# Kernel tuning notes

Hardware: AMD Instinct MI355X
Metric: run time of the kernel (lower is better)

The kernel has to match this reference:

```python
import jax, jax.numpy as jnp
import numpy as np

U = 256      # lstm_unit / embedding_fc_unit
V = 100000   # word vocab
WD = 300     # word embedding dim
PD = 64      # pos embedding dim
AD = 64      # action embedding dim
P = 50       # pos vocab
NA = 164     # 4 + 4*dep_num actions
B, T, K, L, S, A, DQ = 64, 128, 4, 128, 64, 64, 32
FORGET_BIAS = 1.0


def lstm_step(x, c, h, W, b):
    z = jnp.concatenate([x, h], -1) @ W + b
    i, j, f, o = jnp.split(z, 4, -1)
    nc = c * jax.nn.sigmoid(f + FORGET_BIAS) + jax.nn.sigmoid(i) * jnp.tanh(j)
    nh = jnp.tanh(nc) * jax.nn.sigmoid(o)
    return nc, nh


def run_lstm(xs, length, W, b):
    # xs: [B, L, D]; TF dynamic_rnn semantics: state frozen and output zeroed past length.
    Bn, Ln, _ = xs.shape
    u = W.shape[1] // 4
    def step(carry, tx):
        c, h = carry
        t, x = tx
        nc, nh = lstm_step(x, c, h, W, b)
        m = (t < length)[:, None]
        return (jnp.where(m, nc, c), jnp.where(m, nh, h)), jnp.where(m, nh, 0.0)
    init = (jnp.zeros((Bn, u), xs.dtype), jnp.zeros((Bn, u), xs.dtype))
    (cf, hf), outs = jax.lax.scan(step, init, (jnp.arange(Ln), jnp.swapaxes(xs, 0, 1)))
    return jnp.swapaxes(outs, 0, 1), (cf, hf)


def reverse_seq(xs, length):
    # tf.reverse_sequence: reverse first `length` steps, leave the rest in place.
    Ln = xs.shape[1]
    t = jnp.arange(Ln)[None, :]
    rev = jnp.where(t < length[:, None], length[:, None] - 1 - t, t)
    return jnp.take_along_axis(xs, rev[:, :, None], axis=1)


def forward(tree_word_id, tree_pos_id, token_word_id, token_pos_id, history_action_id,
            buff_top_id, deque_word_id, deque_pos_id, deque_length, children_order,
            stack_order, stack_length, token_length, history_action_length,
            word_emb, pos_emb, act_emb, wd_W, wd_b, tree_W, tree_b,
            stack0_W, stack0_b, stack1_W, stack1_b,
            fw0_W, fw0_b, bw0_W, bw0_b, fw1_W, fw1_b, bw1_W, bw1_b,
            act0_W, act0_b, act1_W, act1_b, dq0_W, dq0_b, dq1_W, dq1_b,
            fin_W, fin_b):
    Bn = tree_word_id.shape[0]

    def embed(wid, pid):
        e = jnp.concatenate([word_emb[wid], pos_emb[pid]], -1)
        return jax.nn.relu(e @ wd_W + wd_b)

    tree_e = embed(tree_word_id, tree_pos_id)       # [B, T, U]
    token_e = embed(token_word_id, token_pos_id)    # [B, L, U]
    deque_e = embed(deque_word_id, deque_pos_id)    # [B, DQ, U]
    hist_e = act_emb[history_action_id]             # [B, A, AD]

    # ---- tree LSTM over children structure ----
    Tn = tree_e.shape[1]
    Kn = children_order.shape[2]
    batch_col = jnp.arange(Bn)[:, None]
    H0 = jnp.zeros((Tn + 1, Bn, U), tree_e.dtype)
    C0 = jnp.zeros((Tn + 1, Bn, U), tree_e.dtype)

    def body(carry, i):
        H, C = carry
        idx = children_order[:, i]            # [B, K] indices into slots 0..i
        h = H[idx, batch_col]                 # [B, K, U]
        c = C[idx, batch_col]
        x = tree_e[:, i]                      # [B, U]
        hj = h.sum(1)
        ijo = jnp.concatenate([x, hj], -1) @ tree_W[:, :3 * U] + tree_b[:3 * U]
        xk = jnp.broadcast_to(x[:, None, :], (Bn, Kn, x.shape[-1]))
        f = jnp.concatenate([xk, h], -1) @ tree_W[:, 3 * U:] + tree_b[3 * U:]   # [B, K, U]
        ig, jg, og = jnp.split(ijo, 3, -1)
        nc = (c * jax.nn.sigmoid(f + FORGET_BIAS)).sum(1) + jax.nn.sigmoid(ig) * jnp.tanh(jg)
        nh = jnp.tanh(nc) * jax.nn.sigmoid(og)
        return (H.at[i + 1].set(nh), C.at[i + 1].set(nc)), None

    (H, _), _ = jax.lax.scan(body, (H0, C0), jnp.arange(Tn))
    stack_embedded = H[stack_order, batch_col]      # [B, S, U]

    # ---- stack LSTM (2-layer) ----
    o0, _ = run_lstm(stack_embedded, stack_length, stack0_W, stack0_b)
    _, (_, stack_h) = run_lstm(o0, stack_length, stack1_W, stack1_b)

    # ---- buff bi-LSTM (2 stacked bidirectional layers) ----
    fw0_o, _ = run_lstm(token_e, token_length, fw0_W, fw0_b)
    bw0_o, _ = run_lstm(reverse_seq(token_e, token_length), token_length, bw0_W, bw0_b)
    bw0_o = reverse_seq(bw0_o, token_length)
    x1 = jnp.concatenate([fw0_o, bw0_o], -1)
    fw1_o, (_, fw1_h) = run_lstm(x1, token_length, fw1_W, fw1_b)
    bw1_o, _ = run_lstm(reverse_seq(x1, token_length), token_length, bw1_W, bw1_b)
    bw1_o = reverse_seq(bw1_o, token_length)
    bidx = jnp.arange(Bn)
    fw_top = fw1_o[bidx, buff_top_id]
    bw_top = bw1_o[bidx, buff_top_id]
    bw_bottom = bw1_o[bidx, token_length - 1]
    buff_out = jnp.concatenate([fw1_h - fw_top, bw_top - bw_bottom], -1)

    # ---- action LSTM (2-layer) ----
    a0, _ = run_lstm(hist_e, history_action_length, act0_W, act0_b)
    _, (_, act_h) = run_lstm(a0, history_action_length, act1_W, act1_b)

    # ---- deque LSTM (2-layer) ----
    d0, _ = run_lstm(deque_e, deque_length, dq0_W, dq0_b)
    _, (_, dq_h) = run_lstm(d0, deque_length, dq1_W, dq1_b)

    feat = jnp.concatenate([stack_h, buff_out, act_h, dq_h], -1)   # [B, 5U]
    return jax.nn.relu(feat @ fin_W + fin_b)


def setup_inputs():
    key = jax.random.key(0)
    ks = jax.random.split(key, 48)
    r = lambda i, shape: jax.random.normal(ks[i], shape, jnp.float32) * 0.05
    ri = lambda i, shape, hi: jax.random.randint(ks[i], shape, 0, hi)
    inp = {}
    inp['tree_word_id'] = ri(0, (B, T), V)
    inp['tree_pos_id'] = ri(1, (B, T), P)
    inp['token_word_id'] = ri(2, (B, L), V)
    inp['token_pos_id'] = ri(3, (B, L), P)
    inp['history_action_id'] = ri(4, (B, A), NA)
    inp['buff_top_id'] = ri(5, (B,), L // 2)
    inp['deque_word_id'] = ri(6, (B, DQ), V)
    inp['deque_pos_id'] = ri(7, (B, DQ), P)
    inp['deque_length'] = jax.random.randint(ks[8], (B,), 1, DQ + 1)
    co = ri(9, (B, T, K), T)
    # a node may only reference already-computed children slots (<= step index)
    inp['children_order'] = jnp.minimum(co, jnp.arange(T)[None, :, None])
    inp['stack_order'] = ri(10, (B, S), T + 1)
    inp['stack_length'] = jax.random.randint(ks[11], (B,), 1, S + 1)
    inp['token_length'] = jax.random.randint(ks[12], (B,), L // 2, L + 1)
    inp['history_action_length'] = jax.random.randint(ks[13], (B,), 1, A + 1)
    inp['word_emb'] = r(14, (V, WD))
    inp['pos_emb'] = r(15, (P, PD))
    inp['act_emb'] = r(16, (NA, AD))
    inp['wd_W'] = r(17, (WD + PD, U)); inp['wd_b'] = jnp.zeros((U,))
    inp['tree_W'] = r(18, (2 * U, 4 * U)); inp['tree_b'] = jnp.zeros((4 * U,))
    inp['stack0_W'] = r(19, (2 * U, 4 * U)); inp['stack0_b'] = jnp.zeros((4 * U,))
    inp['stack1_W'] = r(20, (2 * U, 4 * U)); inp['stack1_b'] = jnp.zeros((4 * U,))
    inp['fw0_W'] = r(21, (2 * U, 4 * U)); inp['fw0_b'] = jnp.zeros((4 * U,))
    inp['bw0_W'] = r(22, (2 * U, 4 * U)); inp['bw0_b'] = jnp.zeros((4 * U,))
    inp['fw1_W'] = r(23, (3 * U, 4 * U)); inp['fw1_b'] = jnp.zeros((4 * U,))
    inp['bw1_W'] = r(24, (3 * U, 4 * U)); inp['bw1_b'] = jnp.zeros((4 * U,))
    inp['act0_W'] = r(25, (AD + U, 4 * U)); inp['act0_b'] = jnp.zeros((4 * U,))
    inp['act1_W'] = r(26, (2 * U, 4 * U)); inp['act1_b'] = jnp.zeros((4 * U,))
    inp['dq0_W'] = r(27, (2 * U, 4 * U)); inp['dq0_b'] = jnp.zeros((4 * U,))
    inp['dq1_W'] = r(28, (2 * U, 4 * U)); inp['dq1_b'] = jnp.zeros((4 * U,))
    inp['fin_W'] = r(29, (5 * U, NA)); inp['fin_b'] = jnp.zeros((NA,))
    return inp


def reference(tree_word_id, tree_pos_id, token_word_id, token_pos_id, history_action_id,
              buff_top_id, deque_word_id, deque_pos_id, deque_length, children_order,
              stack_order, stack_length, token_length, history_action_length,
              word_emb, pos_emb, act_emb, wd_W, wd_b, tree_W, tree_b,
              stack0_W, stack0_b, stack1_W, stack1_b,
              fw0_W, fw0_b, bw0_W, bw0_b, fw1_W, fw1_b, bw1_W, bw1_b,
              act0_W, act0_b, act1_W, act1_b, dq0_W, dq0_b, dq1_W, dq1_b,
              fin_W, fin_b):
    return forward(tree_word_id, tree_pos_id, token_word_id, token_pos_id, history_action_id,
                   buff_top_id, deque_word_id, deque_pos_id, deque_length, children_order,
                   stack_order, stack_length, token_length, history_action_length,
                   word_emb, pos_emb, act_emb, wd_W, wd_b, tree_W, tree_b,
                   stack0_W, stack0_b, stack1_W, stack1_b,
                   fw0_W, fw0_b, bw0_W, bw0_b, fw1_W, fw1_b, bw1_W, bw1_b,
                   act0_W, act0_b, act1_W, act1_b, dq0_W, dq0_b, dq1_W, dq1_b,
                   fin_W, fin_b)
```

## Files before the change

### kernel.cpp

```cpp
#include <hip/hip_runtime.h>
#include <hip/hip_bf16.h>
#include <hip/hip_fp16.h>
#include <cstdint>

#define BB   64
#define TT   128
#define KK   4
#define LL   128
#define SS   64
#define AA   64
#define DQN  32
#define UU   256
#define NAOUT 164
#define WDIM 300
#define PDIM 64
#define ADIM 64

#define OFF_TREE 0
#define OFF_S0   512
#define OFF_S1   1024
#define OFF_FW0  1536
#define OFF_BW0  2048
#define OFF_FW1  2560
#define OFF_BW1  3328
#define OFF_ACT0 4096
#define OFF_ACT1 4416
#define OFF_DQ0  4928
#define OFF_DQ1  5440
#define PK_ROWS_FB 5952

#define PKH_FW0  512
#define PKH_BW0  768
#define PKH_FW1  1024
#define PKH_BW1  1280
#define PKH_S0   1536
#define PKH_S1   1792
#define PKH_ACT0 2048
#define PKH_ACT1 2304
#define PKH_DQ0  2560
#define PKH_DQ1  2816
#define PK_ROWS_B 3072

typedef unsigned short ushort_t;
typedef unsigned int   uint_t;

__device__ __forceinline__ float bf2f(ushort_t s) {
    return __uint_as_float(((uint_t)s) << 16);
}
__device__ __forceinline__ ushort_t f2bf(float x) {
    __hip_bfloat16 h = __float2bfloat16(x);
    return *reinterpret_cast<ushort_t*>(&h);
}
__device__ __forceinline__ float sigm(float x) { return 1.0f / (1.0f + expf(-x)); }

__device__ __forceinline__ uint_t pack2h(float a, float b) {
    __half2 h = __floats2half2_rn(a, b);
    return *reinterpret_cast<uint_t*>(&h);
}
__device__ __forceinline__ float2 unp2h(uint_t v) {
    __half2 h = *reinterpret_cast<__half2*>(&v);
    return __half22float2(h);
}

template<bool F32>
__device__ __forceinline__ float ld1(const void* p_, size_t i) {
    if constexpr (F32) return reinterpret_cast<const float*>(p_)[i];
    else               return bf2f(reinterpret_cast<const ushort_t*>(p_)[i]);
}

struct P {
    const int *tree_word_id, *tree_pos_id, *token_word_id, *token_pos_id, *history_action_id,
              *buff_top_id, *deque_word_id, *deque_pos_id, *deque_length, *children_order,
              *stack_order, *stack_length, *token_length, *history_action_length;
    const void *word_emb, *pos_emb, *act_emb, *wd_W, *wd_b, *tree_W, *tree_b,
        *stack0_W, *stack0_b, *stack1_W, *stack1_b, *fw0_W, *fw0_b, *bw0_W, *bw0_b,
        *fw1_W, *fw1_b, *bw1_W, *bw1_b, *act0_W, *act0_b, *act1_W, *act1_b,
        *dq0_W, *dq0_b, *dq1_W, *dq1_b, *fin_W, *fin_b;
    int* flag;
    float *stack_h, *fw1_h, *fw_top, *bw_top, *bw_bottom, *act_h, *dq_h;
    float *tree_e;
    ushort_t *token_e, *deque_e, *x1;
    float *H, *C;
    float *a0_seq, *d0_seq, *s0_seq;
    uint2 *zxA, *zxB, *zxC, *zxD, *zxS;
    float4* pkf;
};

__global__ void detect_kernel(const uint_t* w, int* flag) {
    __shared__ int cnt;
    if (threadIdx.x == 0) cnt = 0;
    __syncthreads();
    int local = 0;
    for (int i = threadIdx.x; i < 256; i += 64) {
        uint_t lo = w[i] & 0xFFFFu;
        uint_t e  = (lo >> 7) & 0xFFu;
        if (lo == 0u || (e >= 0x6Cu && e <= 0x7Fu)) local++;
    }
    atomicAdd(&cnt, local);
    __syncthreads();
    if (threadIdx.x == 0) flag[0] = (cnt >= 200) ? 0 : 1;
}

__global__ void sentinel_kernel(void* out, float v) {
    if (threadIdx.x == 0) {
        reinterpret_cast<float*>(out)[0] = v;
        reinterpret_cast<__hip_bfloat16*>(out)[2] = __float2bfloat16(v);
    }
}

__global__ __launch_bounds__(256) void pack_fb_kernel(P p) {
    const bool f32 = (p.flag[0] == 1);
    const int rg = blockIdx.x;
    const int u  = threadIdx.x;
    const void* src; int r;
    if      (rg < 512)  { src = p.tree_W;   r = rg; }
    else if (rg < 1024) { src = p.stack0_W; r = rg - 512; }
    else if (rg < 1536) { src = p.stack1_W; r = rg - 1024; }
    else if (rg < 2048) { src = p.fw0_W;    r = rg - 1536; }
    else if (rg < 2560) { src = p.bw0_W;    r = rg - 2048; }
    else if (rg < 3328) { src = p.fw1_W;    r = rg - 2560; }
    else if (rg < 4096) { src = p.bw1_W;    r = rg - 3328; }
    else if (rg < 4416) { src = p.act0_W;   r = rg - 4096; }
    else if (rg < 4928) { src = p.act1_W;   r = rg - 4416; }
    else if (rg < 5440) { src = p.dq0_W;    r = rg - 4928; }
    else                { src = p.dq1_W;    r = rg - 5440; }
    const size_t ro = (size_t)r * 1024;
    float4 v;
    if (f32) {
        const float* s = reinterpret_cast<const float*>(src) + ro;
        v = make_float4(s[u], s[256 + u], s[512 + u], s[768 + u]);
    } else {
        const ushort_t* s = reinterpret_cast<const ushort_t*>(src) + ro;
        v = make_float4(bf2f(s[u]), bf2f(s[256 + u]), bf2f(s[512 + u]), bf2f(s[768 + u]));
    }
    p.pkf[(size_t)rg * 256 + u] = v;
}

__global__ __launch_bounds__(256) void pack_h_kernel(P p) {
    const bool f32 = (p.flag[0] == 1);
    const int rg = blockIdx.x;
    const int u  = threadIdx.x;
    const void* src; int r;
    if      (rg < 512)  { src = p.tree_W;   r = rg; }
    else if (rg < 768)  { src = p.fw0_W;    r = 256 + rg - 512; }
    else if (rg < 1024) { src = p.bw0_W;    r = 256 + rg - 768; }
    else if (rg < 1280) { src = p.fw1_W;    r = 512 + rg - 1024; }
    else if (rg < 1536) { src = p.bw1_W;    r = 512 + rg - 1280; }
    else if (rg < 1792) { src = p.stack0_W; r = 256 + rg - 1536; }
    else if (rg < 2048) { src = p.stack1_W; r = 256 + rg - 1792; }
    else if (rg < 2304) { src = p.act0_W;   r = 64  + rg - 2048; }
    else if (rg < 2560) { src = p.act1_W;   r = 256 + rg - 2304; }
    else if (rg < 2816) { src = p.dq0_W;    r = 256 + rg - 2560; }
    else                { src = p.dq1_W;    r = 256 + rg - 2816; }
    const size_t ro = (size_t)r * 1024;
    float4 v;
    if (f32) {
        const float* s = reinterpret_cast<const float*>(src) + ro;
        v = make_float4(s[u], s[256 + u], s[512 + u], s[768 + u]);
    } else {
        const ushort_t* s = reinterpret_cast<const ushort_t*>(src) + ro;
        v = make_float4(bf2f(s[u]), bf2f(s[256 + u]), bf2f(s[512 + u]), bf2f(s[768 + u]));
    }
    p.pkf[(size_t)rg * 256 + u] = v;
}

template<bool F32>
__device__ void embed_impl(const P& p, float* s_e) {
    const int u   = threadIdx.x;
// ... 316 lines not shown
    s_xh[512 + u] = 0.f;
    for (int t = 0; t < len; ++t) {
        const int row = is_bw ? (len - 1 - t) : t;
        const ushort_t* xr = p.x1 + ((size_t)b * LL + row) * 512;
        s_xh[u]       = bf2f(xr[u]);
        s_xh[256 + u] = bf2f(xr[256 + u]);
        __syncthreads();
        const float nh = lstm_step_f4<768>(Wp, bz, s_xh, c1);
        if (!is_bw) {
            if (t == btop) p.fw_top[b * UU + u] = nh;
        } else {
            if (t == 0)              p.bw_bottom[b * UU + u] = nh;
            if (t == len - 1 - btop) p.bw_top[b * UU + u]    = nh;
        }
        __syncthreads();
        s_xh[512 + u] = nh;
        hlast = nh;
    }
    if (!is_bw) p.fw1_h[b * UU + u] = hlast;
}

__global__ __launch_bounds__(256) void phase2_fb_kernel(P p) {
    __shared__ __align__(16) float smem[1024];
    const bool f32 = (p.flag[0] == 1);
    const int chain = blockIdx.x % 3;
    const int b     = blockIdx.x / 3;
    if (f32) {
        if (chain == 0)      run_stack_f4<true>(b, p, smem);
        else if (chain == 1) run_token_l1_f4<true>(b, p, smem, false);
        else                 run_token_l1_f4<true>(b, p, smem, true);
    } else {
        if (chain == 0)      run_stack_f4<false>(b, p, smem);
        else if (chain == 1) run_token_l1_f4<false>(b, p, smem, false);
        else                 run_token_l1_f4<false>(b, p, smem, true);
    }
}

template<bool F32, int R>
__device__ void xpre_compute(const void* __restrict__ W, const void* __restrict__ bias,
                             uint2* __restrict__ zx, int n0,
                             const float* __restrict__ s_xf, const ushort_t* __restrict__ s_xb) {
    const int u = threadIdx.x;
    const float4 bz = load_bias4<F32>(bias, u);
    for (int c = 0; c < 32; c += 8) {
        float4 acc[8];
        #pragma unroll
        for (int n = 0; n < 8; ++n) acc[n] = bz;
        for (int r0 = 0; r0 < R; r0 += 8) {
            float4 w[8];
            #pragma unroll
            for (int k = 0; k < 8; ++k) {
                const size_t ro = (size_t)(r0 + k) * 1024;
                w[k] = make_float4(ld1<F32>(W, ro + u),
                                   ld1<F32>(W, ro + 256 + u),
                                   ld1<F32>(W, ro + 512 + u),
                                   ld1<F32>(W, ro + 768 + u));
            }
            #pragma unroll
            for (int n = 0; n < 8; ++n) {
                float xv[8];
                #pragma unroll
                for (int k = 0; k < 8; ++k)
                    xv[k] = (R == 512) ? bf2f(s_xb[(size_t)(c + n) * 512 + r0 + k])
                                       : s_xf[(size_t)(c + n) * R + r0 + k];
                #pragma unroll
                for (int k = 0; k < 8; ++k) {
                    acc[n].x = fmaf(xv[k], w[k].x, acc[n].x);
                    acc[n].y = fmaf(xv[k], w[k].y, acc[n].y);
                    acc[n].z = fmaf(xv[k], w[k].z, acc[n].z);
                    acc[n].w = fmaf(xv[k], w[k].w, acc[n].w);
                }
            }
        }
        #pragma unroll
        for (int n = 0; n < 8; ++n) {
            uint2 v;
            v.x = pack2h(acc[n].x, acc[n].y);
            v.y = pack2h(acc[n].z, acc[n].w);
            zx[(size_t)(n0 + c + n) * 256 + u] = v;
        }
    }
}

template<bool F32, int STAGE>
__device__ void xpre_impl(const P& p, char* s_raw) {
    float*    s_xf = reinterpret_cast<float*>(s_raw);
    ushort_t* s_xb = reinterpret_cast<ushort_t*>(s_raw);
    const int blk = blockIdx.x;
    const int tid = threadIdx.x;

    const void* W; const void* bias; uint2* zx; int R; int kind; int n0;
    if (STAGE == 0) {
        if (blk < 256)      { W=p.fw0_W;  bias=p.fw0_b;  zx=p.zxA; R=256; kind=0; n0=blk*32; }
        else if (blk < 512) { W=p.bw0_W;  bias=p.bw0_b;  zx=p.zxB; R=256; kind=0; n0=(blk-256)*32; }
        else if (blk < 640) { W=p.act0_W; bias=p.act0_b; zx=p.zxC; R=64;  kind=3; n0=(blk-512)*32; }
        else                { W=p.dq0_W;  bias=p.dq0_b;  zx=p.zxD; R=256; kind=1; n0=(blk-640)*32; }
    } else if (STAGE == 1) {
        if (blk < 256)      { W=p.fw1_W;    bias=p.fw1_b;    zx=p.zxA; R=512; kind=2; n0=blk*32; }
        else if (blk < 512) { W=p.bw1_W;    bias=p.bw1_b;    zx=p.zxB; R=512; kind=2; n0=(blk-256)*32; }
        else if (blk < 640) { W=p.stack0_W; bias=p.stack0_b; zx=p.zxS; R=256; kind=4; n0=(blk-512)*32; }
        else if (blk < 768) { W=p.act1_W;   bias=p.act1_b;   zx=p.zxC; R=256; kind=5; n0=(blk-640)*32; }
        else                { W=p.dq1_W;    bias=p.dq1_b;    zx=p.zxD; R=256; kind=6; n0=(blk-768)*32; }
    } else {
        W=p.stack1_W; bias=p.stack1_b; zx=p.zxS; R=256; kind=7; n0=blk*32;
    }

    if (kind == 0 || kind == 1) {
        const ushort_t* src = (kind == 0 ? p.token_e : p.deque_e) + (size_t)n0 * 256;
        for (int i = tid; i < 32 * 256; i += 256) s_xf[i] = bf2f(src[i]);
    } else if (kind == 2) {
        const ushort_t* src = p.x1 + (size_t)n0 * 512;
        for (int i = tid; i < 32 * 512; i += 256) s_xb[i] = src[i];
    } else if (kind == 3) {
        const int b = n0 >> 6, t0 = n0 & 63;
        for (int i = tid; i < 32 * 64; i += 256) {
            const int t = t0 + (i >> 6), r = i & 63;
            int aid = p.history_action_id[b * AA + t];
            aid = aid < 0 ? 0 : (aid > NAOUT - 1 ? NAOUT - 1 : aid);
            s_xf[i] = ld1<F32>(p.act_emb, (size_t)aid * ADIM + r);
        }
    } else if (kind == 4) {
        const int b = n0 >> 6, t0 = n0 & 63;
        for (int i = tid; i < 32 * 256; i += 256) {
            const int t = t0 + (i >> 8), r = i & 255;
            int so = p.stack_order[b * SS + t];
            so = so < 0 ? 0 : (so > TT ? TT : so);
            s_xf[i] = p.H[((size_t)so * BB + b) * UU + r];
        }
    } else {
        const float* src = (kind == 5 ? p.a0_seq : kind == 6 ? p.d0_seq : p.s0_seq)
                         + (size_t)n0 * 256;
        for (int i = tid; i < 32 * 256; i += 256) s_xf[i] = src[i];
    }
    __syncthreads();

    if (R == 512)      xpre_compute<F32, 512>(W, bias, zx, n0, s_xf, s_xb);
    else if (R == 256) xpre_compute<F32, 256>(W, bias, zx, n0, s_xf, s_xb);
    else               xpre_compute<F32, 64 >(W, bias, zx, n0, s_xf, s_xb);
}

__global__ __launch_bounds__(256) void xpre0_kernel(P p) {
    __shared__ __align__(16) char s_raw[32768];
    if (p.flag[0] == 1) xpre_impl<true, 0>(p, s_raw);
    else                xpre_impl<false, 0>(p, s_raw);
}
__global__ __launch_bounds__(256) void xpre1_kernel(P p) {
    __shared__ __align__(16) char s_raw[32768];
    if (p.flag[0] == 1) xpre_impl<true, 1>(p, s_raw);
    else                xpre_impl<false, 1>(p, s_raw);
}
__global__ __launch_bounds__(256) void xpre2_kernel(P p) {
    __shared__ __align__(16) char s_raw[32768];
    if (p.flag[0] == 1) xpre_impl<true, 2>(p, s_raw);
    else                xpre_impl<false, 2>(p, s_raw);
}

template<bool F32>
__device__ void p1_impl(const P& p, float* smem) {
    const int chain = blockIdx.x >> 6;
    const int b     = blockIdx.x & 63;
    if (chain == 0) { run_tree_f4<F32>(b, p, smem); return; }

    const int u = threadIdx.x;
    float* s_h = smem;
    float c = 0.f;
    s_h[u] = 0.f;
    __syncthreads();

    if (chain == 1 || chain == 2) {
        const bool bw = (chain == 2);
        const int len = p.token_length[b];
        const float4* __restrict__ Wh = p.pkf + (size_t)(bw ? PKH_BW0 : PKH_FW0) * 256 + u;
        const uint2* zx = bw ? p.zxB : p.zxA;
        for (int t = 0; t < len; ++t) {
            const int row = bw ? (len - 1 - t) : t;
            const float4 bz = zx_load(zx, (size_t)b * LL + row, u);
            const float nh = lstm_step_f4<256>(Wh, bz, s_h, c);
            p.x1[((size_t)b * LL + row) * 512 + (bw ? 256 : 0) + u] = f2bf(nh);
            __syncthreads();
            s_h[u] = nh;
            __syncthreads();
        }
    } else if (chain == 3) {
        const int len = p.history_action_length[b];
        const float4* __restrict__ Wh = p.pkf + (size_t)PKH_ACT0 * 256 + u;
        for (int t = 0; t < len; ++t) {
            const float4 bz = zx_load(p.zxC, (size_t)b * AA + t, u);
            const float nh = lstm_step_f4<256>(Wh, bz, s_h, c);
            p.a0_seq[((size_t)b * AA + t) * UU + u] = nh;
            __syncthreads();
            s_h[u] = nh;
            __syncthreads();
        }
    } else {
        const int len = p.deque_length[b];
        const float4* __restrict__ Wh = p.pkf + (size_t)PKH_DQ0 * 256 + u;
        for (int t = 0; t < len; ++t) {
            const float4 bz = zx_load(p.zxD, (size_t)b * DQN + t, u);
            const float nh = lstm_step_f4<256>(Wh, bz, s_h, c);
            p.d0_seq[((size_t)b * DQN + t) * UU + u] = nh;
            __syncthreads();
            s_h[u] = nh;
            __syncthreads();
        }
    }
}

__global__ __launch_bounds__(256) void p1_kernel(P p) {
    __shared__ __align__(16) float smem[1536];
    if (p.flag[0] == 1) p1_impl<true>(p, smem);
    else                p1_impl<false>(p, smem);
}

template<bool F32>
__device__ void p2_impl(const P& p, float* smem) {
    const int chain = blockIdx.x >> 6;
    const int b     = blockIdx.x & 63;
    const int u = threadIdx.x;
    float* s_h = smem;
    float c = 0.f;
    s_h[u] = 0.f;
    __syncthreads();

    if (chain == 0) {
        const int len  = p.token_length[b];
        const int btop = p.buff_top_id[b];
        const float4* __restrict__ Wh = p.pkf + (size_t)PKH_FW1 * 256 + u;
        float hlast = 0.f;
        for (int t = 0; t < len; ++t) {
            const float4 bz = zx_load(p.zxA, (size_t)b * LL + t, u);
            const float nh = lstm_step_f4<256>(Wh, bz, s_h, c);
            if (t == btop) p.fw_top[b * UU + u] = nh;
            __syncthreads();
            s_h[u] = nh;
            __syncthreads();
            hlast = nh;
        }
        p.fw1_h[b * UU + u] = hlast;
    } else if (chain == 1) {
        const int len  = p.token_length[b];
        const int btop = p.buff_top_id[b];
        const float4* __restrict__ Wh = p.pkf + (size_t)PKH_BW1 * 256 + u;
        for (int t = 0; t < len; ++t) {
            const int row = len - 1 - t;
            const float4 bz = zx_load(p.zxB, (size_t)b * LL + row, u);
            const float nh = lstm_step_f4<256>(Wh, bz, s_h, c);
            if (t == 0)              p.bw_bottom[b * UU + u] = nh;
            if (t == len - 1 - btop) p.bw_top[b * UU + u]    = nh;
            __syncthreads();
            s_h[u] = nh;
            __syncthreads();
        }
    } else if (chain == 2) {
        const int len = p.stack_length[b];
        const float4* __restrict__ Wh = p.pkf + (size_t)PKH_S0 * 256 + u;
        for (int t = 0; t < len; ++t) {
            const float4 bz = zx_load(p.zxS, (size_t)b * SS + t, u);
            const float nh = lstm_step_f4<256>(Wh, bz, s_h, c);
            p.s0_seq[((size_t)b * SS + t) * UU + u] = nh;
            __syncthreads();
            s_h[u] = nh;
            __syncthreads();
        }
    } else if (chain == 3) {
        const int len = p.history_action_length[b];
        const float4* __restrict__ Wh = p.pkf + (size_t)PKH_ACT1 * 256 + u;
        float hlast = 0.f;
        for (int t = 0; t < len; ++t) {
            const float4 bz = zx_load(p.zxC, (size_t)b * AA + t, u);
            const float nh = lstm_step_f4<256>(Wh, bz, s_h, c);
            __syncthreads();
            s_h[u] = nh;
            __syncthreads();
            hlast = nh;
        }
        p.act_h[b * UU + u] = hlast;
    } else {
        const int len = p.deque_length[b];
        const float4* __restrict__ Wh = p.pkf + (size_t)PKH_DQ1 * 256 + u;
        float hlast = 0.f;
        for (int t = 0; t < len; ++t) {
            const float4 bz = zx_load(p.zxD, (size_t)b * DQN + t, u);
            const float nh = lstm_step_f4<256>(Wh, bz, s_h, c);
            __syncthreads();
            s_h[u] = nh;
            __syncthreads();
            hlast = nh;
        }
        p.dq_h[b * UU + u] = hlast;
    }
}

__global__ __launch_bounds__(256) void p2_kernel(P p) {
    __shared__ __align__(16) float smem[256];
    if (p.flag[0] == 1) p2_impl<true>(p, smem);
    else                p2_impl<false>(p, smem);
}

template<bool F32>
__device__ void p3_impl(const P& p, float* smem) {
    const int b = blockIdx.x;
    const int u = threadIdx.x;
    float* s_h = smem;
    float c = 0.f;
    s_h[u] = 0.f;
    __syncthreads();
    const int len = p.stack_length[b];
    const float4* __restrict__ Wh = p.pkf + (size_t)PKH_S1 * 256 + u;
    float hlast = 0.f;
    for (int t = 0; t < len; ++t) {
        const float4 bz = zx_load(p.zxS, (size_t)b * SS + t, u);
        const float nh = lstm_step_f4<256>(Wh, bz, s_h, c);
        __syncthreads();
        s_h[u] = nh;
        __syncthreads();
        hlast = nh;
    }
    p.stack_h[b * UU + u] = hlast;
}

__global__ __launch_bounds__(256) void p3_kernel(P p) {
    __shared__ __align__(16) float smem[256];
    if (p.flag[0] == 1) p3_impl<true>(p, smem);
    else                p3_impl<false>(p, smem);
}

template<bool F32>
__device__ __forceinline__ void st_out(void* out, int i, float v) {
    if constexpr (F32) reinterpret_cast<float*>(out)[i] = v;
    else               reinterpret_cast<__hip_bfloat16*>(out)[i] = __float2bfloat16(v);
}

template<bool F32>
__device__ void final_impl(const P& p, void* out, float* s_f) {
    const int b = blockIdx.x;
    const int u = threadIdx.x;
    s_f[u]        = p.stack_h[b * UU + u];
    s_f[256 + u]  = p.fw1_h[b * UU + u] - p.fw_top[b * UU + u];
    s_f[512 + u]  = p.bw_top[b * UU + u] - p.bw_bottom[b * UU + u];
    s_f[768 + u]  = p.act_h[b * UU + u];
    s_f[1024 + u] = p.dq_h[b * UU + u];
    __syncthreads();
    if (u < NAOUT) {
        float acc = ld1<F32>(p.fin_b, u);
        for (int r = 0; r < 1280; ++r)
            acc = fmaf(s_f[r], ld1<F32>(p.fin_W, (size_t)r * NAOUT + u), acc);
        acc = fmaxf(acc, 0.f);
        st_out<F32>(out, b * NAOUT + u, acc);
    }
    if (b == 0 && u == 0) {
        const uint_t POIS = 0xAAAAAAAAu;
        const uint_t* te = reinterpret_cast<const uint_t*>(p.tree_e);
        const uint_t* x1 = reinterpret_cast<const uint_t*>(p.x1);
        const uint_t* sh = reinterpret_cast<const uint_t*>(p.stack_h);
        bool te_p = true, x1_p = true;
        for (int i = 0; i < 8; ++i) { te_p &= (te[i] == POIS); x1_p &= (x1[i] == POIS); }
        bool sh_p = (sh[0] == POIS) && (sh[1] == POIS);
        float sent = 0.f;
        if (te_p)      sent = 3000.f;
        else if (x1_p) sent = 4000.f;
        else if (sh_p) sent = 5000.f;
        else if (*reinterpret_cast<const uint_t*>(p.flag) == POIS) sent = 6000.f;
        if (sent > 0.f) st_out<F32>(out, 0, sent);
    }
}

__global__ __launch_bounds__(256) void final_kernel(P p, void* out) {
    __shared__ __align__(16) float s_f[1280];
    if (p.flag[0] == 1) final_impl<true>(p, out, s_f);
    else                final_impl<false>(p, out, s_f);
}

extern "C" void kernel_launch(void* const* d_in, const int* in_sizes, int n_in,
                              void* d_out, int out_size, void* d_ws, size_t ws_size,
                              hipStream_t stream) {
    if (n_in != 43) {
        sentinel_kernel<<<1, 64, 0, stream>>>(d_out, 9000.f + (float)n_in);
        return;
    }
    if (out_size != NAOUT * BB) {
        sentinel_kernel<<<1, 64, 0, stream>>>(d_out, 8000.f);
        return;
    }

    P p;
    p.tree_word_id          = (const int*)d_in[0];
    p.tree_pos_id           = (const int*)d_in[1];
    p.token_word_id         = (const int*)d_in[2];
    p.token_pos_id          = (const int*)d_in[3];
    p.history_action_id     = (const int*)d_in[4];
    p.buff_top_id           = (const int*)d_in[5];
    p.deque_word_id         = (const int*)d_in[6];
    p.deque_pos_id          = (const int*)d_in[7];
    p.deque_length          = (const int*)d_in[8];
    p.children_order        = (const int*)d_in[9];
    p.stack_order           = (const int*)d_in[10];
    p.stack_length          = (const int*)d_in[11];
    p.token_length          = (const int*)d_in[12];
    p.history_action_length = (const int*)d_in[13];
    p.word_emb = d_in[14];
    p.pos_emb  = d_in[15];
    p.act_emb  = d_in[16];
    p.wd_W     = d_in[17];
    p.wd_b     = d_in[18];
    p.tree_W   = d_in[19];
    p.tree_b   = d_in[20];
    p.stack0_W = d_in[21];
    p.stack0_b = d_in[22];
    p.stack1_W = d_in[23];
    p.stack1_b = d_in[24];
    p.fw0_W    = d_in[25];
    p.fw0_b    = d_in[26];
    p.bw0_W    = d_in[27];
    p.bw0_b    = d_in[28];
    p.fw1_W    = d_in[29];
    p.fw1_b    = d_in[30];
    p.bw1_W    = d_in[31];
    p.bw1_b    = d_in[32];
    p.act0_W   = d_in[33];
    p.act0_b   = d_in[34];
    p.act1_W   = d_in[35];
    p.act1_b   = d_in[36];
    p.dq0_W    = d_in[37];
    p.dq0_b    = d_in[38];
    p.dq1_W    = d_in[39];
    p.dq1_b    = d_in[40];
    p.fin_W    = d_in[41];
    p.fin_b    = d_in[42];

    char* base = (char*)d_ws;

    size_t off = 0;
    p.flag = (int*)(base + off);           off += 256;
    p.stack_h   = (float*)(base + off);    off += (size_t)BB * UU * 4;
    p.fw1_h     = (float*)(base + off);    off += (size_t)BB * UU * 4;
    p.fw_top    = (float*)(base + off);    off += (size_t)BB * UU * 4;
    p.bw_top    = (float*)(base + off);    off += (size_t)BB * UU * 4;
    p.bw_bottom = (float*)(base + off);    off += (size_t)BB * UU * 4;
    p.act_h     = (float*)(base + off);    off += (size_t)BB * UU * 4;
    p.dq_h      = (float*)(base + off);    off += (size_t)BB * UU * 4;
    p.tree_e  = (float*)(base + off);      off += (size_t)BB * TT * UU * 4;
    p.token_e = (ushort_t*)(base + off);   off += (size_t)BB * LL * UU * 2;
    p.deque_e = (ushort_t*)(base + off);   off += (size_t)BB * DQN * UU * 2;
    p.x1      = (ushort_t*)(base + off);   off += (size_t)BB * LL * 512 * 2;
    p.a0_seq  = (float*)(base + off);      off += (size_t)BB * AA * UU * 4;
    p.d0_seq  = (float*)(base + off);      off += (size_t)BB * DQN * UU * 4;
    p.s0_seq  = (float*)(base + off);      off += (size_t)BB * SS * UU * 4;
    p.H       = (float*)(base + off);      off += (size_t)(TT + 1) * BB * UU * 4;
    p.C       = (float*)(base + off);      off += (size_t)(TT + 1) * BB * UU * 4;
    p.zxA     = (uint2*)(base + off);      off += (size_t)BB * LL * UU * 8;
    p.zxB     = (uint2*)(base + off);      off += (size_t)BB * LL * UU * 8;
    p.zxC     = (uint2*)(base + off);      off += (size_t)BB * AA * UU * 8;
    p.zxD     = (uint2*)(base + off);      off += (size_t)BB * DQN * UU * 8;
    p.zxS     = (uint2*)(base + off);      off += (size_t)BB * SS * UU * 8;
    p.pkf     = (float4*)(base + off);     off += (size_t)PK_ROWS_B * 256 * 16;
    const size_t planB_size = off;

    if (ws_size >= planB_size) {
        detect_kernel<<<1, 64, 0, stream>>>((const uint_t*)d_in[14], p.flag);
        pack_h_kernel<<<dim3(PK_ROWS_B), dim3(256), 0, stream>>>(p);
        embed_kernel<<<dim3(BB * TT + BB * LL + BB * DQN), dim3(256), 0, stream>>>(p);
        xpre0_kernel<<<dim3(704), dim3(256), 0, stream>>>(p);
        p1_kernel<<<dim3(5 * BB), dim3(256), 0, stream>>>(p);
        xpre1_kernel<<<dim3(832), dim3(256), 0, stream>>>(p);
        p2_kernel<<<dim3(5 * BB), dim3(256), 0, stream>>>(p);
        xpre2_kernel<<<dim3(128), dim3(256), 0, stream>>>(p);
        p3_kernel<<<dim3(BB), dim3(256), 0, stream>>>(p);
        final_kernel<<<dim3(BB), dim3(256), 0, stream>>>(p, d_out);
        return;
    }

    off = 0;
    p.flag = (int*)(base + off);           off += 16;
    p.stack_h   = (float*)(base + off);    off += (size_t)BB * UU * 4;
    p.fw1_h     = (float*)(base + off);    off += (size_t)BB * UU * 4;
    p.fw_top    = (float*)(base + off);    off += (size_t)BB * UU * 4;
    p.bw_top    = (float*)(base + off);    off += (size_t)BB * UU * 4;
    p.bw_bottom = (float*)(base + off);    off += (size_t)BB * UU * 4;
    p.act_h     = (float*)(base + off);    off += (size_t)BB * UU * 4;
    p.dq_h      = (float*)(base + off);    off += (size_t)BB * UU * 4;
    p.tree_e  = (float*)(base + off);      off += (size_t)BB * TT * UU * 4;
    p.token_e = (ushort_t*)(base + off);   off += (size_t)BB * LL * UU * 2;
    p.deque_e = (ushort_t*)(base + off);   off += (size_t)BB * DQN * UU * 2;
    p.x1      = (ushort_t*)(base + off);   off += (size_t)BB * LL * 512 * 2;
    p.H       = (float*)(base + off);      off += (size_t)(TT + 1) * BB * UU * 4;
    p.C       = (float*)(base + off);      off += (size_t)(TT + 1) * BB * UU * 4;
    p.pkf     = (float4*)(base + off);     off += (size_t)PK_ROWS_FB * 256 * 16;
    p.a0_seq = p.d0_seq = p.s0_seq = (float*)base;
    p.zxA = p.zxB = p.zxC = p.zxD = p.zxS = (uint2*)base;

    if (ws_size < off) {
        sentinel_kernel<<<1, 64, 0, stream>>>(d_out, 7000.f + (float)(ws_size >> 20));
        return;
    }

    detect_kernel<<<1, 64, 0, stream>>>((const uint_t*)d_in[14], p.flag);
    pack_fb_kernel<<<dim3(PK_ROWS_FB), dim3(256), 0, stream>>>(p);
    embed_kernel<<<dim3(BB * TT + BB * LL + BB * DQN), dim3(256), 0, stream>>>(p);
    phase1_fb_kernel<<<dim3(4 * BB), dim3(256), 0, stream>>>(p);
    phase2_fb_kernel<<<dim3(3 * BB), dim3(256), 0, stream>>>(p);
    final_kernel<<<dim3(BB), dim3(256), 0, stream>>>(p, d_out);
}
```

Baseline: 6.336 ms.

## Split recurrent LSTM chains into per-timestep grid launches across units and batch

Replaces the persistent per-batch-row recurrent kernels (one block per sequence running all timesteps) with one kernel launch per timestep. Each launch spreads the hidden units and batch rows over 256 blocks, with hidden and cell state kept in global double-buffered arrays. The tree LSTM's input projection is moved into the xpre0 GEMM stage (new zxT buffer), so each tree step only does the recurrent part. The aim is to use many more CUs per step and share weight loads across batch rows. The cost is hundreds of kernel launches and a global-memory round trip for state on every step.

```diff
diff --git a/kernel.cpp b/kernel.cpp
--- a/kernel.cpp
+++ b/kernel.cpp
@@ -83,7 +83,10 @@
     float *H, *C;
     float *a0_seq, *d0_seq, *s0_seq;
     uint2 *zxA, *zxB, *zxC, *zxD, *zxS;
+    float4* zxT;
     float4* pkf;
+    float *hs;
+    float *cs;
 };
 
 __global__ void detect_kernel(const uint_t* w, int* flag) {
@@ -566,6 +569,46 @@
     }
 }
 
+template<bool F32>
+__device__ void xpre_tree_compute(const void* __restrict__ W, const void* __restrict__ bias,
+                                  float4* __restrict__ zxT, int n0,
+                                  const float* __restrict__ s_xf) {
+    const int u = threadIdx.x;
+    const float4 bz = make_float4(ld1<F32>(bias, u), ld1<F32>(bias, 256 + u),
+                                  ld1<F32>(bias, 512 + u),
+                                  ld1<F32>(bias, 768 + u) + 1.0f);
+    for (int c = 0; c < 32; c += 8) {
+        float4 acc[8];
+        #pragma unroll
+        for (int n = 0; n < 8; ++n) acc[n] = bz;
+        for (int r0 = 0; r0 < 256; r0 += 8) {
+            float4 w[8];
+            #pragma unroll
+            for (int k = 0; k < 8; ++k) {
+                const size_t ro = (size_t)(r0 + k) * 1024;
+                w[k] = make_float4(ld1<F32>(W, ro + u),
+                                   ld1<F32>(W, ro + 256 + u),
+                                   ld1<F32>(W, ro + 512 + u),
+                                   ld1<F32>(W, ro + 768 + u));
+            }
+            #pragma unroll
+            for (int n = 0; n < 8; ++n) {
+                #pragma unroll
+                for (int k = 0; k < 8; ++k) {
+                    const float xv = s_xf[(size_t)(c + n) * 256 + r0 + k];
+                    acc[n].x = fmaf(xv, w[k].x, acc[n].x);
+                    acc[n].y = fmaf(xv, w[k].y, acc[n].y);
+                    acc[n].z = fmaf(xv, w[k].z, acc[n].z);
+                    acc[n].w = fmaf(xv, w[k].w, acc[n].w);
+                }
+            }
+        }
+        #pragma unroll
+        for (int n = 0; n < 8; ++n)
+            zxT[(size_t)(n0 + c + n) * 256 + u] = acc[n];
+    }
+}
+
 template<bool F32, int STAGE>
 __device__ void xpre_impl(const P& p, char* s_raw) {
     float*    s_xf = reinterpret_cast<float*>(s_raw);
@@ -573,12 +616,13 @@
     const int blk = blockIdx.x;
     const int tid = threadIdx.x;
 
-    const void* W; const void* bias; uint2* zx; int R; int kind; int n0;
+    const void* W; const void* bias; uint2* zx = nullptr; int R; int kind; int n0;
     if (STAGE == 0) {
         if (blk < 256)      { W=p.fw0_W;  bias=p.fw0_b;  zx=p.zxA; R=256; kind=0; n0=blk*32; }
         else if (blk < 512) { W=p.bw0_W;  bias=p.bw0_b;  zx=p.zxB; R=256; kind=0; n0=(blk-256)*32; }
         else if (blk < 640) { W=p.act0_W; bias=p.act0_b; zx=p.zxC; R=64;  kind=3; n0=(blk-512)*32; }
-        else                { W=p.dq0_W;  bias=p.dq0_b;  zx=p.zxD; R=256; kind=1; n0=(blk-640)*32; }
+        else if (blk < 704) { W=p.dq0_W;  bias=p.dq0_b;  zx=p.zxD; R=256; kind=1; n0=(blk-640)*32; }
+        else                { W=p.tree_W; bias=p.tree_b; R=256;    kind=8; n0=(blk-704)*32; }
     } else if (STAGE == 1) {
         if (blk < 256)      { W=p.fw1_W;    bias=p.fw1_b;    zx=p.zxA; R=512; kind=2; n0=blk*32; }
         else if (blk < 512) { W=p.bw1_W;    bias=p.bw1_b;    zx=p.zxB; R=512; kind=2; n0=(blk-256)*32; }
@@ -611,6 +655,9 @@
             so = so < 0 ? 0 : (so > TT ? TT : so);
             s_xf[i] = p.H[((size_t)so * BB + b) * UU + r];
         }
+    } else if (kind == 8) {
+        const float* src = p.tree_e + (size_t)n0 * 256;
+        for (int i = tid; i < 32 * 256; i += 256) s_xf[i] = src[i];
     } else {
         const float* src = (kind == 5 ? p.a0_seq : kind == 6 ? p.d0_seq : p.s0_seq)
                          + (size_t)n0 * 256;
@@ -618,7 +665,8 @@
     }
     __syncthreads();
 
-    if (R == 512)      xpre_compute<F32, 512>(W, bias, zx, n0, s_xf, s_xb);
+    if (kind == 8)     xpre_tree_compute<F32>(W, bias, p.zxT, n0, s_xf);
+    else if (R == 512) xpre_compute<F32, 512>(W, bias, zx, n0, s_xf, s_xb);
     else if (R == 256) xpre_compute<F32, 256>(W, bias, zx, n0, s_xf, s_xb);
     else               xpre_compute<F32, 64 >(W, bias, zx, n0, s_xf, s_xb);
 }
@@ -639,174 +687,220 @@
     else                xpre_impl<false, 2>(p, s_raw);
 }
 
-template<bool F32>
-__device__ void p1_impl(const P& p, float* smem) {
-    const int chain = blockIdx.x >> 6;
-    const int b     = blockIdx.x & 63;
-    if (chain == 0) { run_tree_f4<F32>(b, p, smem); return; }
-
-    const int u = threadIdx.x;
-    float* s_h = smem;
-    float c = 0.f;
-    s_h[u] = 0.f;
+
+__global__ void init_hc_kernel(P p) {
+    const int b = blockIdx.x, u = threadIdx.x;
+    p.H[(size_t)b * UU + u] = 0.f;
+    p.C[(size_t)b * UU + u] = 0.f;
+}
+
+__device__ __forceinline__ float* h_buf(const P& p, int ch, int parity) {
+    return p.hs + (size_t)(ch * 2 + parity) * (64 * 256);
+}
+__device__ __forceinline__ float* c_buf(const P& p, int ch) {
+    return p.cs + (size_t)ch * (64 * 256);
+}
+
+__device__ __forceinline__ void chain_out(const P& p, int kind, int b, int u,
+                                          int t, int len, int row, float nh) {
+    switch (kind) {
+    case 0: p.x1[((size_t)b * LL + row) * 512 + u]       = f2bf(nh); break;
+    case 1: p.x1[((size_t)b * LL + row) * 512 + 256 + u] = f2bf(nh); break;
+    case 2: p.a0_seq[((size_t)b * AA + t) * UU + u]  = nh; break;
+    case 3: p.d0_seq[((size_t)b * DQN + t) * UU + u] = nh; break;
+    case 4:
+        if (t == p.buff_top_id[b]) p.fw_top[b * UU + u] = nh;
+        if (t == len - 1)          p.fw1_h[b * UU + u]  = nh;
+        break;
+    case 5:
+        if (t == 0)                          p.bw_bottom[b * UU + u] = nh;
+        if (t == len - 1 - p.buff_top_id[b]) p.bw_top[b * UU + u]    = nh;
+        break;
+    case 6: p.s0_seq[((size_t)b * SS + t) * UU + u] = nh; break;
+    case 7: if (t == len - 1) p.act_h[b * UU + u]   = nh; break;
+    case 8: if (t == len - 1) p.dq_h[b * UU + u]    = nh; break;
+    default: if (t == len - 1) p.stack_h[b * UU + u] = nh; break;
+    }
+}
+
+__device__ void step_hchain(const P& p, int t, int kind, int u0, int b0, float* sH) {
+    const int tid = threadIdx.x;
+    const uint2* zx; const int* lenarr; int zs; int base;
+    switch (kind) {
+    case 0: zx = p.zxA; lenarr = p.token_length;          zs = LL;  base = PKH_FW0;  break;
+    case 1: zx = p.zxB; lenarr = p.token_length;          zs = LL;  base = PKH_BW0;  break;
+    case 2: zx = p.zxC; lenarr = p.history_action_length; zs = AA;  base = PKH_ACT0; break;
+    case 3: zx = p.zxD; lenarr = p.deque_length;          zs = DQN; base = PKH_DQ0;  break;
+    case 4: zx = p.zxA; lenarr = p.token_length;          zs = LL;  base = PKH_FW1;  break;
+    case 5: zx = p.zxB; lenarr = p.token_length;          zs = LL;  base = PKH_BW1;  break;
+    case 6: zx = p.zxS; lenarr = p.stack_length;          zs = SS;  base = PKH_S0;   break;
+    case 7: zx = p.zxC; lenarr = p.history_action_length; zs = AA;  base = PKH_ACT1; break;
+    case 8: zx = p.zxD; lenarr = p.deque_length;          zs = DQN; base = PKH_DQ1;  break;
+    default: zx = p.zxS; lenarr = p.stack_length;         zs = SS;  base = PKH_S1;   break;
+    }
+
+    if (t == 0) {
+        for (int idx = tid; idx < 8192; idx += 256) sH[idx] = 0.f;
+    } else {
+        const float* hr = h_buf(p, kind, t & 1);
+        for (int idx = tid; idx < 8192; idx += 256) {
+            const int bb = idx >> 8, r = idx & 255;
+            sH[idx] = hr[(size_t)(b0 + bb) * 256 + r];
+        }
+    }
     __syncthreads();
 
-    if (chain == 1 || chain == 2) {
-        const bool bw = (chain == 2);
-        const int len = p.token_length[b];
-        const float4* __restrict__ Wh = p.pkf + (size_t)(bw ? PKH_BW0 : PKH_FW0) * 256 + u;
-        const uint2* zx = bw ? p.zxB : p.zxA;
-        for (int t = 0; t < len; ++t) {
-            const int row = bw ? (len - 1 - t) : t;
-            const float4 bz = zx_load(zx, (size_t)b * LL + row, u);
-            const float nh = lstm_step_f4<256>(Wh, bz, s_h, c);
-            p.x1[((size_t)b * LL + row) * 512 + (bw ? 256 : 0) + u] = f2bf(nh);
-            __syncthreads();
-            s_h[u] = nh;
-            __syncthreads();
-        }
-    } else if (chain == 3) {
-        const int len = p.history_action_length[b];
-        const float4* __restrict__ Wh = p.pkf + (size_t)PKH_ACT0 * 256 + u;
-        for (int t = 0; t < len; ++t) {
-            const float4 bz = zx_load(p.zxC, (size_t)b * AA + t, u);
-            const float nh = lstm_step_f4<256>(Wh, bz, s_h, c);
-            p.a0_seq[((size_t)b * AA + t) * UU + u] = nh;
-            __syncthreads();
-            s_h[u] = nh;
-            __syncthreads();
-        }
-    } else {
-        const int len = p.deque_length[b];
-        const float4* __restrict__ Wh = p.pkf + (size_t)PKH_DQ0 * 256 + u;
-        for (int t = 0; t < len; ++t) {
-            const float4 bz = zx_load(p.zxD, (size_t)b * DQN + t, u);
-            const float nh = lstm_step_f4<256>(Wh, bz, s_h, c);
-            p.d0_seq[((size_t)b * DQN + t) * UU + u] = nh;
-            __syncthreads();
-            s_h[u] = nh;
-            __syncthreads();
-        }
-    }
-}
-
-__global__ __launch_bounds__(256) void p1_kernel(P p) {
-    __shared__ __align__(16) float smem[1536];
-    if (p.flag[0] == 1) p1_impl<true>(p, smem);
-    else                p1_impl<false>(p, smem);
-}
-
-template<bool F32>
-__device__ void p2_impl(const P& p, float* smem) {
-    const int chain = blockIdx.x >> 6;
-    const int b     = blockIdx.x & 63;
-    const int u = threadIdx.x;
-    float* s_h = smem;
-    float c = 0.f;
-    s_h[u] = 0.f;
+    const int u  = u0 + (tid & 15);
+    const int q  = tid >> 4;
+    const int bA = b0 + 2 * q, bBt = bA + 1;
+    const int lenA = lenarr[bA], lenB = lenarr[bBt];
+    const bool aA = (t < lenA), aB = (t < lenB);
+    int rowA = t, rowB = t;
+    if (kind == 1 || kind == 5) {
+        rowA = aA ? (lenA - 1 - t) : 0;
+        rowB = aB ? (lenB - 1 - t) : 0;
+    }
+    float4 accA = zx_load(zx, (size_t)bA * zs + rowA, u);
+    float4 accB = zx_load(zx, (size_t)bBt * zs + rowB, u);
+
+    const float4* __restrict__ Wh = p.pkf + (size_t)base * 256 + u;
+    const float* hA = sH + (2 * q) * 256;
+    const float* hB = hA + 256;
+    for (int r0 = 0; r0 < 256; r0 += 8) {
+        float4 w[8];
+        #pragma unroll
+        for (int k = 0; k < 8; ++k) w[k] = Wh[(size_t)(r0 + k) * 256];
+        __builtin_amdgcn_sched_barrier(0);
+        #pragma unroll
+        for (int k = 0; k < 8; ++k) {
+            const float xA = hA[r0 + k], xB = hB[r0 + k];
+            accA.x = fmaf(xA, w[k].x, accA.x);
+            accA.y = fmaf(xA, w[k].y, accA.y);
+            accA.z = fmaf(xA, w[k].z, accA.z);
+            accA.w = fmaf(xA, w[k].w, accA.w);
+            accB.x = fmaf(xB, w[k].x, accB.x);
+            accB.y = fmaf(xB, w[k].y, accB.y);
+            accB.z = fmaf(xB, w[k].z, accB.z);
+            accB.w = fmaf(xB, w[k].w, accB.w);
+        }
+    }
+
+    float* cst = c_buf(p, kind);
+    float* hw  = h_buf(p, kind, (t + 1) & 1);
+    {
+        float nh;
+        if (aA) {
+            const float c = (t == 0) ? 0.f : cst[(size_t)bA * 256 + u];
+            const float nc = c * sigm(accA.z) + sigm(accA.x) * tanhf(accA.y);
+            cst[(size_t)bA * 256 + u] = nc;
+            nh = tanhf(nc) * sigm(accA.w);
+            chain_out(p, kind, bA, u, t, lenA, rowA, nh);
+        } else {
+            nh = hA[u];
+        }
+        hw[(size_t)bA * 256 + u] = nh;
+    }
+    {
+        float nh;
+        if (aB) {
+            const float c = (t == 0) ? 0.f : cst[(size_t)bBt * 256 + u];
+            const float nc = c * sigm(accB.z) + sigm(accB.x) * tanhf(accB.y);
+            cst[(size_t)bBt * 256 + u] = nc;
+            nh = tanhf(nc) * sigm(accB.w);
+            chain_out(p, kind, bBt, u, t, lenB, rowB, nh);
+        } else {
+            nh = hB[u];
+        }
+        hw[(size_t)bBt * 256 + u] = nh;
+    }
+}
+
+__device__ void step_tree(const P& p, int t, int u0, int b0, float* sm) {
+    const int tid = threadIdx.x;
+    for (int idx = tid; idx < 16384; idx += 256) {
+        const int r = idx & 255, k = (idx >> 8) & 3, bbs = idx >> 10;
+        const int b = b0 + bbs;
+        const int co = p.children_order[((size_t)b * TT + t) * KK + k];
+        sm[idx] = p.H[((size_t)co * BB + b) * UU + r];
+    }
     __syncthreads();
 
-    if (chain == 0) {
-        const int len  = p.token_length[b];
-        const int btop = p.buff_top_id[b];
-        const float4* __restrict__ Wh = p.pkf + (size_t)PKH_FW1 * 256 + u;
-        float hlast = 0.f;
-        for (int t = 0; t < len; ++t) {
-            const float4 bz = zx_load(p.zxA, (size_t)b * LL + t, u);
-            const float nh = lstm_step_f4<256>(Wh, bz, s_h, c);
-            if (t == btop) p.fw_top[b * UU + u] = nh;
-            __syncthreads();
-            s_h[u] = nh;
-            __syncthreads();
-            hlast = nh;
-        }
-        p.fw1_h[b * UU + u] = hlast;
-    } else if (chain == 1) {
-        const int len  = p.token_length[b];
-        const int btop = p.buff_top_id[b];
-        const float4* __restrict__ Wh = p.pkf + (size_t)PKH_BW1 * 256 + u;
-        for (int t = 0; t < len; ++t) {
-            const int row = len - 1 - t;
-            const float4 bz = zx_load(p.zxB, (size_t)b * LL + row, u);
-            const float nh = lstm_step_f4<256>(Wh, bz, s_h, c);
-            if (t == 0)              p.bw_bottom[b * UU + u] = nh;
-            if (t == len - 1 - btop) p.bw_top[b * UU + u]    = nh;
-            __syncthreads();
-            s_h[u] = nh;
-            __syncthreads();
-        }
-    } else if (chain == 2) {
-        const int len = p.stack_length[b];
-        const float4* __restrict__ Wh = p.pkf + (size_t)PKH_S0 * 256 + u;
-        for (int t = 0; t < len; ++t) {
-            const float4 bz = zx_load(p.zxS, (size_t)b * SS + t, u);
-            const float nh = lstm_step_f4<256>(Wh, bz, s_h, c);
-            p.s0_seq[((size_t)b * SS + t) * UU + u] = nh;
-            __syncthreads();
-            s_h[u] = nh;
-            __syncthreads();
-        }
-    } else if (chain == 3) {
-        const int len = p.history_action_length[b];
-        const float4* __restrict__ Wh = p.pkf + (size_t)PKH_ACT1 * 256 + u;
-        float hlast = 0.f;
-        for (int t = 0; t < len; ++t) {
-            const float4 bz = zx_load(p.zxC, (size_t)b * AA + t, u);
-            const float nh = lstm_step_f4<256>(Wh, bz, s_h, c);
-            __syncthreads();
-            s_h[u] = nh;
-            __syncthreads();
-            hlast = nh;
-        }
-        p.act_h[b * UU + u] = hlast;
-    } else {
-        const int len = p.deque_length[b];
-        const float4* __restrict__ Wh = p.pkf + (size_t)PKH_DQ1 * 256 + u;
-        float hlast = 0.f;
-        for (int t = 0; t < len; ++t) {
-            const float4 bz = zx_load(p.zxD, (size_t)b * DQN + t, u);
-            const float nh = lstm_step_f4<256>(Wh, bz, s_h, c);
-            __syncthreads();
-            s_h[u] = nh;
-            __syncthreads();
-            hlast = nh;
-        }
-        p.dq_h[b * UU + u] = hlast;
-    }
-}
-
-__global__ __launch_bounds__(256) void p2_kernel(P p) {
-    __shared__ __align__(16) float smem[256];
-    if (p.flag[0] == 1) p2_impl<true>(p, smem);
-    else                p2_impl<false>(p, smem);
-}
-
-template<bool F32>
-__device__ void p3_impl(const P& p, float* smem) {
-    const int b = blockIdx.x;
-    const int u = threadIdx.x;
-    float* s_h = smem;
-    float c = 0.f;
-    s_h[u] = 0.f;
-    __syncthreads();
-    const int len = p.stack_length[b];
-    const float4* __restrict__ Wh = p.pkf + (size_t)PKH_S1 * 256 + u;
-    float hlast = 0.f;
-    for (int t = 0; t < len; ++t) {
-        const float4 bz = zx_load(p.zxS, (size_t)b * SS + t, u);
-        const float nh = lstm_step_f4<256>(Wh, bz, s_h, c);
-        __syncthreads();
-        s_h[u] = nh;
-        __syncthreads();
-        hlast = nh;
-    }
-    p.stack_h[b * UU + u] = hlast;
-}
-
-__global__ __launch_bounds__(256) void p3_kernel(P p) {
-    __shared__ __align__(16) float smem[256];
-    if (p.flag[0] == 1) p3_impl<true>(p, smem);
-    else                p3_impl<false>(p, smem);
+    const int u = u0 + (tid & 15);
+    const int bb = tid >> 4;
+    const int b = b0 + bb;
+    const float4 z0 = p.zxT[((size_t)b * TT + t) * 256 + u];
+    float zi = z0.x, zj = z0.y, zo = z0.z, fx = z0.w;
+    float f0 = 0.f, f1 = 0.f, f2 = 0.f, f3 = 0.f;
+    const float4* __restrict__ Wh = p.pkf + (size_t)256 * 256 + u;
+    const float* hkb = sm + bb * 1024;
+    for (int r0 = 0; r0 < 256; r0 += 8) {
+        float4 w[8];
+        #pragma unroll
+        for (int k = 0; k < 8; ++k) w[k] = Wh[(size_t)(r0 + k) * 256];
+        __builtin_amdgcn_sched_barrier(0);
+        #pragma unroll
+        for (int k = 0; k < 8; ++k) {
+            const int r = r0 + k;
+            const float k0 = hkb[r], k1 = hkb[256 + r], k2 = hkb[512 + r], k3 = hkb[768 + r];
+            const float hj = k0 + k1 + k2 + k3;
+            zi = fmaf(hj, w[k].x, zi);
+            zj = fmaf(hj, w[k].y, zj);
+            zo = fmaf(hj, w[k].z, zo);
+            f0 = fmaf(k0, w[k].w, f0);
+            f1 = fmaf(k1, w[k].w, f1);
+            f2 = fmaf(k2, w[k].w, f2);
+            f3 = fmaf(k3, w[k].w, f3);
+        }
+    }
+    float cc[4];
+    #pragma unroll
+    for (int k = 0; k < 4; ++k) {
+        const int co = p.children_order[((size_t)b * TT + t) * KK + k];
+        cc[k] = p.C[((size_t)co * BB + b) * UU + u];
+    }
+    const float fsum = cc[0] * sigm(fx + f0) + cc[1] * sigm(fx + f1)
+                     + cc[2] * sigm(fx + f2) + cc[3] * sigm(fx + f3);
+    const float nc = fsum + sigm(zi) * tanhf(zj);
+    const float nh = tanhf(nc) * sigm(zo);
+    p.H[((size_t)(t + 1) * BB + b) * UU + u] = nh;
+    p.C[((size_t)(t + 1) * BB + b) * UU + u] = nc;
+}
+
+__global__ __launch_bounds__(256) void p1step_kernel(P p, int t) {
+    __shared__ __align__(16) float sm[16384];
+    const int s = blockIdx.x & 7;
+    const int j = blockIdx.x >> 3;
+    if (s <= 1) {
+        step_tree(p, t, (j & 15) * 16, (((s << 1) | (j >> 4))) * 16, sm);
+        return;
+    }
+    int kind;
+    if (s == 2)      kind = 0;
+    else if (s == 3) kind = 1;
+    else if (s == 4) { if (t >= AA)  return; kind = 2; }
+    else if (s == 5) { if (t >= DQN) return; kind = 3; }
+    else return;
+    step_hchain(p, t, kind, (j & 15) * 16, (j >> 4) * 32, sm);
+}
+
+__global__ __launch_bounds__(256) void p2step_kernel(P p, int t) {
+    __shared__ __align__(16) float sm[8192];
+    const int s = blockIdx.x & 7;
+    const int j = blockIdx.x >> 3;
+    int kind;
+    if (s == 0)      kind = 4;
+    else if (s == 1) kind = 5;
+    else if (s == 2) { if (t >= SS)  return; kind = 6; }
+    else if (s == 3) { if (t >= AA)  return; kind = 7; }
+    else if (s == 4) { if (t >= DQN) return; kind = 8; }
+    else return;
+    step_hchain(p, t, kind, (j & 15) * 16, (j >> 4) * 32, sm);
+}
+
+__global__ __launch_bounds__(256) void p3step_kernel(P p, int t) {
+    __shared__ __align__(16) float sm[8192];
+    const int j = blockIdx.x;
+    step_hchain(p, t, 9, (j & 15) * 16, (j >> 4) * 32, sm);
 }
 
 template<bool F32>
@@ -834,15 +928,13 @@
     }
     if (b == 0 && u == 0) {
         const uint_t POIS = 0xAAAAAAAAu;
-        const uint_t* te = reinterpret_cast<const uint_t*>(p.tree_e);
         const uint_t* x1 = reinterpret_cast<const uint_t*>(p.x1);
         const uint_t* sh = reinterpret_cast<const uint_t*>(p.stack_h);
-        bool te_p = true, x1_p = true;
-        for (int i = 0; i < 8; ++i) { te_p &= (te[i] == POIS); x1_p &= (x1[i] == POIS); }
+        bool x1_p = true;
+        for (int i = 0; i < 8; ++i) x1_p &= (x1[i] == POIS);
         bool sh_p = (sh[0] == POIS) && (sh[1] == POIS);
         float sent = 0.f;
-        if (te_p)      sent = 3000.f;
-        else if (x1_p) sent = 4000.f;
+        if (x1_p)      sent = 4000.f;
         else if (sh_p) sent = 5000.f;
         else if (*reinterpret_cast<const uint_t*>(p.flag) == POIS) sent = 6000.f;
         if (sent > 0.f) st_out<F32>(out, 0, sent);
@@ -938,18 +1030,25 @@
     p.zxD     = (uint2*)(base + off);      off += (size_t)BB * DQN * UU * 8;
     p.zxS     = (uint2*)(base + off);      off += (size_t)BB * SS * UU * 8;
     p.pkf     = (float4*)(base + off);     off += (size_t)PK_ROWS_B * 256 * 16;
-    const size_t planB_size = off;
-
-    if (ws_size >= planB_size) {
+    p.zxT     = (float4*)(base + off);     off += (size_t)BB * TT * UU * 16;
+    const size_t planE_size = off;
+    p.hs = (float*)p.tree_e;
+    p.cs = p.hs + (size_t)10 * 2 * 64 * 256;
+
+    if (ws_size >= planE_size) {
         detect_kernel<<<1, 64, 0, stream>>>((const uint_t*)d_in[14], p.flag);
         pack_h_kernel<<<dim3(PK_ROWS_B), dim3(256), 0, stream>>>(p);
         embed_kernel<<<dim3(BB * TT + BB * LL + BB * DQN), dim3(256), 0, stream>>>(p);
-        xpre0_kernel<<<dim3(704), dim3(256), 0, stream>>>(p);
-        p1_kernel<<<dim3(5 * BB), dim3(256), 0, stream>>>(p);
+        init_hc_kernel<<<dim3(BB), dim3(256), 0, stream>>>(p);
+        xpre0_kernel<<<dim3(960), dim3(256), 0, stream>>>(p);
+        for (int t = 0; t < TT; ++t)
+            p1step_kernel<<<dim3(256), dim3(256), 0, stream>>>(p, t);
         xpre1_kernel<<<dim3(832), dim3(256), 0, stream>>>(p);
-        p2_kernel<<<dim3(5 * BB), dim3(256), 0, stream>>>(p);
+        for (int t = 0; t < LL; ++t)
+            p2step_kernel<<<dim3(256), dim3(256), 0, stream>>>(p, t);
         xpre2_kernel<<<dim3(128), dim3(256), 0, stream>>>(p);
-        p3_kernel<<<dim3(BB), dim3(256), 0, stream>>>(p);
+        for (int t = 0; t < SS; ++t)
+            p3step_kernel<<<dim3(32), dim3(256), 0, stream>>>(p, t);
         final_kernel<<<dim3(BB), dim3(256), 0, stream>>>(p, d_out);
         return;
     }
@@ -972,6 +1071,8 @@
     p.pkf     = (float4*)(base + off);     off += (size_t)PK_ROWS_FB * 256 * 16;
     p.a0_seq = p.d0_seq = p.s0_seq = (float*)base;
     p.zxA = p.zxB = p.zxC = p.zxD = p.zxS = (uint2*)base;
+    p.zxT = (float4*)base;
+    p.hs = p.cs = (float*)base;
 
     if (ws_size < off) {
         sentinel_kernel<<<1, 64, 0, stream>>>(d_out, 7000.f + (float)(ws_size >> 20));
```

Result: slower. 7.334 ms (+15.8%).
